# Kernel tuning notes

Hardware: AMD Instinct MI355X
Metric: run time of the kernel (lower is better)

Reference implementation:

```python
import jax, jax.numpy as jnp
import numpy as np

B, T, D, H = 8, 1024, 512, 8
DK = D // H


def setup_inputs() -> dict:
    key = jax.random.key(0)
    ks = jax.random.split(key, 6)
    s = 0.02
    return {
        "inputs": jax.random.normal(ks[0], (B, T, D), jnp.float32),
        "ln1_g": jnp.ones((D,), jnp.float32),
        "ln1_b": jnp.zeros((D,), jnp.float32),
        "ln2_g": jnp.ones((D,), jnp.float32),
        "ln2_b": jnp.zeros((D,), jnp.float32),
        "W_qkv": jax.random.normal(ks[1], (3 * D, D), jnp.float32) * s,
        "W_pos": jax.random.normal(ks[2], (D, D), jnp.float32) * s,
        "W_out": jax.random.normal(ks[3], (D, D), jnp.float32) * s,
        "b_out": jnp.zeros((D,), jnp.float32),
        "pos_bias_u": jax.random.normal(ks[4], (H, DK), jnp.float32) * s,
        "pos_bias_v": jax.random.normal(ks[5], (H, DK), jnp.float32) * s,
    }


def layer_norm(x, g, b, eps=1e-5):
    mu = jnp.mean(x, axis=-1, keepdims=True)
    var = jnp.var(x, axis=-1, keepdims=True)
    return (x - mu) * jax.lax.rsqrt(var + eps) * g + b


def rel_shift(x):
    # x: (b, h, t1, t2); Transformer-XL pad-reshape-slice relative shift
    b, h, t1, t2 = x.shape
    xp = jnp.pad(x, ((0, 0), (0, 0), (0, 0), (1, 0)))  # zero col at front
    xp = xp.reshape(b, h, t2 + 1, t1)[:, :, 1:, :]
    return xp.reshape(b, h, t1, t2)


def reference(inputs, ln1_g, ln1_b, ln2_g, ln2_b, W_qkv, W_pos, W_out, b_out,
              pos_bias_u, pos_bias_v):
    b, t, d = inputs.shape
    # PositionalEmbedding: pos_seq is the literal data values inputs[0,:,0]
    pos_seq = inputs[0, :, 0]
    inv_freq = 1.0 / (10000.0 ** (jnp.arange(0, d, 2, dtype=jnp.float32) / d))
    sin_inp = pos_seq[:, None] * inv_freq[None, :]  # (T, D/2)
    pos_emb = jnp.concatenate([jnp.sin(sin_inp), jnp.cos(sin_inp)], axis=-1)  # (T, D)
    # outer layer norm, then inner layer norm inside forward_qkv
    x = layer_norm(inputs, ln1_g, ln1_b)
    xn = layer_norm(x, ln2_g, ln2_b)
    qkv = xn @ W_qkv.T  # (B, T, 3D)
    q, k, v = jnp.split(qkv, 3, axis=-1)
    q = q.reshape(b, t, H, DK)                       # (B, T, H, DK)
    k = k.reshape(b, t, H, DK).transpose(0, 2, 1, 3)  # (B, H, T, DK)
    v = v.reshape(b, t, H, DK).transpose(0, 2, 1, 3)  # (B, H, T, DK)
    p = (pos_emb @ W_pos.T).reshape(t, H, DK)         # (T, H, DK), pos batch = 1
    qu = (q + pos_bias_u).transpose(0, 2, 1, 3)       # (B, H, T, DK)
    qv = (q + pos_bias_v).transpose(0, 2, 1, 3)
    ac = jnp.einsum('bhqd,bhkd->bhqk', qu, k)
    bd = jnp.einsum('bhqd,khd->bhqk', qv, p)
    bd = rel_shift(bd)
    scores = (ac + bd) / jnp.sqrt(jnp.float32(DK))
    attn = jax.nn.softmax(scores, axis=-1)
    out = jnp.einsum('bhqk,bhkd->bqhd', attn, v).reshape(b, t, d)
    return out @ W_out.T + b_out
```

## Files before the change

### kernel.cpp

```cpp
#include <hip/hip_runtime.h>
#include <stdint.h>

#define B_ 8
#define T_ 1024
#define D_ 512
#define H_ 8
#define DK_ 64
#define M_ (B_*T_)

#define PREP_CAST_BLKS (5 * D_ * D_ / 4 / 256)
#define PREP_POS_BLKS  (T_)
#define PREP_LN_BLKS   (M_)
#define PREP_BLKS      (PREP_CAST_BLKS + PREP_POS_BLKS + PREP_LN_BLKS)

typedef unsigned short u16;
typedef __attribute__((ext_vector_type(8))) short bf16x8;
typedef __attribute__((ext_vector_type(4))) float f32x4;

static __device__ __forceinline__ u16 f2bf(float f) {
  union { float f; unsigned u; } v; v.f = f;
  unsigned r = (v.u + 0x7fffu + ((v.u >> 16) & 1u)) >> 16;
  return (u16)r;
}
static __device__ __forceinline__ u16 f2bf_ru(float f) {
  union { float f; unsigned u; } v; v.f = f;
  return (u16)((v.u + 0x8000u) >> 16);
}
static __device__ __forceinline__ float bf2f(u16 u) {
  union { unsigned u; float f; } v; v.u = ((unsigned)u) << 16;
  return v.f;
}
static __device__ __forceinline__ void async16(const u16* g, u16* l) {
  __builtin_amdgcn_global_load_lds(
      (const __attribute__((address_space(1))) void*)g,
      (__attribute__((address_space(3))) void*)l, 16, 0, 0);
}
static __device__ __forceinline__ f32x4 mfma16(bf16x8 a, bf16x8 b, f32x4 c) {
  return __builtin_amdgcn_mfma_f32_16x16x32_bf16(a, b, c, 0, 0, 0);
}

__global__ __launch_bounds__(256)
void prep_k(const float* __restrict__ wq, const float* __restrict__ wp,
            const float* __restrict__ wo, u16* __restrict__ dq,
            u16* __restrict__ dp, u16* __restrict__ dwo,
            const float* __restrict__ x, u16* __restrict__ pe,
            const float* __restrict__ g1, const float* __restrict__ b1,
            const float* __restrict__ g2, const float* __restrict__ b2,
            u16* __restrict__ xn) {
  __shared__ float red[16];
  const int blk = blockIdx.x;
  const int t = threadIdx.x;
  if (blk < PREP_CAST_BLKS) {
    const int na = 3 * D_ * D_ / 4, nb = D_ * D_ / 4;
    int i = blk * 256 + t;
    const float* s; u16* d; int j;
    if (i < na) { s = wq; d = dq; j = i; }
    else if (i < na + nb) { s = wp; d = dp; j = i - na; }
    else { s = wo; d = dwo; j = i - na - nb; }
    float4 v = ((const float4*)s)[j];
    ushort4 o;
    o.x = f2bf(v.x); o.y = f2bf(v.y); o.z = f2bf(v.z); o.w = f2bf(v.w);
    ((ushort4*)d)[j] = o;
  } else if (blk < PREP_CAST_BLKS + PREP_POS_BLKS) {
    const int tt = blk - PREP_CAST_BLKS;
    float pos = x[(size_t)tt * D_];
    float invf = expf(-(2.f * t / (float)D_) * 9.210340371976184f);
    float ang = pos * invf;
    pe[(size_t)tt * D_ + t] = f2bf(sinf(ang));
    pe[(size_t)tt * D_ + 256 + t] = f2bf(cosf(ang));
  } else {
    const int row = blk - PREP_CAST_BLKS - PREP_POS_BLKS;
    const float2 v = *(const float2*)(x + (size_t)row * D_ + t * 2);
    float a = v.x + v.y;
    float b = v.x * v.x + v.y * v.y;
    for (int off = 32; off; off >>= 1) { a += __shfl_down(a, off, 64); b += __shfl_down(b, off, 64); }
    if ((t & 63) == 0) { red[t >> 6] = a; red[8 + (t >> 6)] = b; }
    __syncthreads();
    a = red[0] + red[1] + red[2] + red[3];
    b = red[8] + red[9] + red[10] + red[11];
    float mu = a * (1.f / D_);
    float var = b * (1.f / D_) - mu * mu;
    float rs = rsqrtf(var + 1e-5f);
    const float2 g1v = *(const float2*)(g1 + t * 2);
    const float2 b1v = *(const float2*)(b1 + t * 2);
    float y0 = (v.x - mu) * rs * g1v.x + b1v.x;
    float y1 = (v.y - mu) * rs * g1v.y + b1v.y;
    __syncthreads();
    a = y0 + y1;
    b = y0 * y0 + y1 * y1;
    for (int off = 32; off; off >>= 1) { a += __shfl_down(a, off, 64); b += __shfl_down(b, off, 64); }
    if ((t & 63) == 0) { red[t >> 6] = a; red[8 + (t >> 6)] = b; }
    __syncthreads();
    a = red[0] + red[1] + red[2] + red[3];
    b = red[8] + red[9] + red[10] + red[11];
    mu = a * (1.f / D_);
    var = b * (1.f / D_) - mu * mu;
    rs = rsqrtf(var + 1e-5f);
    const float2 g2v = *(const float2*)(g2 + t * 2);
    const float2 b2v = *(const float2*)(b2 + t * 2);
    u16* o = xn + (size_t)row * D_ + t * 2;
    o[0] = f2bf((y0 - mu) * rs * g2v.x + b2v.x);
    o[1] = f2bf((y1 - mu) * rs * g2v.y + b2v.y);
  }
}

template<int MODE>
__global__ __launch_bounds__(256, 2)
void gemm_k(const u16* __restrict__ A, const u16* __restrict__ Bw,
            int M, int N, int K,
            u16* __restrict__ o0, u16* __restrict__ o1, u16* __restrict__ o2,
            float* __restrict__ fo, const float* __restrict__ bo) {
  __shared__ u16 As[2][128 * 32];
  __shared__ u16 Bs[2][128 * 32];
  const int tid = threadIdx.x;
  const int l = tid & 63, w = tid >> 6;
  const int m0 = blockIdx.x * 128, n0 = blockIdx.y * 128;
  const int wm = (w >> 1) * 64, wn = (w & 1) * 64;
  const int nk = K >> 5;

  auto stage = [&](int bufi, int kt) {
    const int row = tid >> 2;
    const int cg = ((tid & 3) ^ ((row + (row >> 2)) & 3)) * 8;
    const u16* ga = A + (size_t)(m0 + row) * K + kt * 32 + cg;
    u16* la = &As[bufi][tid * 8];
    async16(ga, la);
    async16(ga + (size_t)64 * K, la + 64 * 32);
    const u16* gb = Bw + (size_t)(n0 + row) * K + kt * 32 + cg;
    u16* lb = &Bs[bufi][tid * 8];
    async16(gb, lb);
    async16(gb + (size_t)64 * K, lb + 64 * 32);
  };

  const int fl = (((l & 15) + ((l & 15) >> 2)) & 3);
  const int coff = ((l >> 4) ^ fl) * 8;
  const int aoff = (l & 15) * 32 + coff;

  f32x4 acc[4][4] = {};
  stage(0, 0);
  for (int kt = 0; kt < nk; ++kt) {
    __syncthreads();
    if (kt + 1 < nk) stage((kt + 1) & 1, kt + 1);
    const u16* as = As[kt & 1];
    const u16* bs = Bs[kt & 1];
    bf16x8 af[4], bfr[4];
#pragma unroll
    for (int i = 0; i < 4; ++i)
      af[i] = *(const bf16x8*)&as[(wm + i * 16) * 32 + aoff];
#pragma unroll
    for (int j = 0; j < 4; ++j)
      bfr[j] = *(const bf16x8*)&bs[(wn + j * 16) * 32 + aoff];
#pragma unroll
    for (int i = 0; i < 4; ++i)
#pragma unroll
      for (int j = 0; j < 4; ++j)
        acc[i][j] = mfma16(af[i], bfr[j], acc[i][j]);
  }

#pragma unroll
  for (int i = 0; i < 4; ++i)
#pragma unroll
    for (int j = 0; j < 4; ++j) {
      const int row0 = m0 + wm + i * 16 + ((l >> 4) << 2);
      const int col = n0 + wn + j * 16 + (l & 15);
      if (MODE == 0) {
        const int sec = col >> 9, cc = col & 511;
        const int hh = cc >> 6, dk = cc & 63;
        const int bb = row0 >> 10, t0r = row0 & 1023;
        if (sec == 2) {
          ushort4 v4;
          v4.x = f2bf(acc[i][j][0]); v4.y = f2bf(acc[i][j][1]);
          v4.z = f2bf(acc[i][j][2]); v4.w = f2bf(acc[i][j][3]);
          *(ushort4*)&o2[((size_t)(bb * H_ + hh) * DK_ + dk) * T_ + t0r] = v4;
        } else {
          u16* dst = (sec == 0) ? o0 : o1;
#pragma unroll
          for (int r = 0; r < 4; ++r)
            dst[((size_t)(bb * H_ + hh) * T_ + t0r + r) * DK_ + dk] = f2bf(acc[i][j][r]);
        }
      } else if (MODE == 1) {
        const int hh = col >> 6, dk = col & 63;
#pragma unroll
        for (int r = 0; r < 4; ++r)
          o0[((size_t)hh * T_ + row0 + r) * DK_ + dk] = f2bf(acc[i][j][r]);
      } else {
#pragma unroll
        for (int r = 0; r < 4; ++r)
          fo[(size_t)(row0 + r) * D_ + col] = acc[i][j][r] + bo[col];
      }
    }
}

__global__ __launch_bounds__(256, 3)
void attn_k(const u16* __restrict__ q, const u16* __restrict__ kb,
            const u16* __restrict__ vt, const u16* __restrict__ pb,
            const float* __restrict__ bu, const float* __restrict__ bv,
            u16* __restrict__ ao) {
  __shared__ u16 k_lds[64 * 64];
  __shared__ u16 v_lds[64 * 64];
  __shared__ u16 p_lds[128 * 64];
  __shared__ float scr[4][16 * 83];

  const int tid = threadIdx.x;
  const int l = tid & 63, w = tid >> 6;
  const int dd = blockIdx.x;
  const int bh = (dd & 7) * 8 + (dd >> 7);
  const int qb = (dd >> 3) & 15;
  const int q0 = qb * 64;
  const int b = bh >> 3, h = bh & 7;

  const u16* qB = q + (size_t)bh * T_ * DK_;
  const u16* kB = kb + (size_t)bh * T_ * DK_;
  const u16* vB = vt + (size_t)bh * DK_ * T_;
  const u16* pB = pb + (size_t)h * T_ * DK_;

  const float SCALE = 0.125f * 1.4426950408889634f;

  bf16x8 quf[2], qvf[2], qsf[2];
  {
    const float* buH = bu + h * DK_;
    const float* bvH = bv + h * DK_;
    const int row = q0 + w * 16 + (l & 15);
    const int row2 = (row + 1 < T_) ? row + 1 : T_ - 1;
    const int ko = (l >> 4) * 8;
    const bf16x8 qa0 = *(const bf16x8*)(qB + (size_t)row * DK_ + ko);
    const bf16x8 qa1 = *(const bf16x8*)(qB + (size_t)row * DK_ + ko + 32);
    const bf16x8 qs0 = *(const bf16x8*)(qB + (size_t)row2 * DK_ + ko);
    const bf16x8 qs1 = *(const bf16x8*)(qB + (size_t)row2 * DK_ + ko + 32);
#pragma unroll
    for (int jj = 0; jj < 8; ++jj) {
      float f0 = bf2f((u16)qa0[jj]), f1 = bf2f((u16)qa1[jj]);
      float g0 = bf2f((u16)qs0[jj]), g1 = bf2f((u16)qs1[jj]);
      float u0 = buH[ko + jj], u1 = buH[ko + 32 + jj];
      float v0 = bvH[ko + jj], v1 = bvH[ko + 32 + jj];
      quf[0][jj] = (short)f2bf((f0 + u0) * SCALE);
      quf[1][jj] = (short)f2bf((f1 + u1) * SCALE);
      qvf[0][jj] = (short)f2bf((f0 + v0) * SCALE);
      qvf[1][jj] = (short)f2bf((f1 + v1) * SCALE);
      qsf[0][jj] = (short)f2bf((g0 + v0) * SCALE);
      qsf[1][jj] = (short)f2bf((g1 + v1) * SCALE);
    }
  }

  f32x4 o[4] = {};
  float lrun[4] = {0.f, 0.f, 0.f, 0.f};
  float sv[4][4];

  const int rbase = 48 - w * 16;
  float* bandf = &scr[w][0];
  u16* pwv = (u16*)&scr[w][0];
  const int lrow = l & 15;
  const int c0s = ((l >> 4) ^ (l & 7)) * 8;
  const int c1s = c0s ^ 32;
  const int qrow0 = (l >> 4) * 4;

  for (int it = 0; it <= 16; ++it) {
    const int kt = it - (it > qb ? 1 : 0);
    const bool phaseU = (it > qb);
    const bool repeat = (it == qb + 1);
    const bool partial = (it == qb);
    const bool needMask = (it >= qb) && (it <= qb + 2);
    const int k0 = kt * 64;
    const int rr0 = tid >> 3;
    const int cg8 = ((tid & 7) ^ (rr0 & 7)) * 8;

    __syncthreads();
    if (!repeat) {
      const u16* g = kB + (size_t)(k0 + rr0) * DK_ + cg8;
      u16* s = &k_lds[tid * 8];
      async16(g, s);
      async16(g + 32 * DK_, s + 32 * 64);
      const u16* g2 = vB + (size_t)rr0 * T_ + k0 + cg8;
      u16* s2 = &v_lds[tid * 8];
      async16(g2, s2);
      async16(g2 + 32 * T_, s2 + 32 * 64);
    }
    {
      const int jb = phaseU ? (k0 - q0 - 65) : (T_ - 64 + k0 - q0);
#pragma unroll
      for (int i = 0; i < 4; ++i) {
        int rr = i * 32 + rr0;
        int j = jb + rr; j = j < 0 ? 0 : (j > T_ - 1 ? T_ - 1 : j);
        async16(pB + (size_t)j * DK_ + cg8, &p_lds[rr * 64 + (tid & 7) * 8]);
      }
    }
    __syncthreads();

    if (!repeat) {
      __builtin_amdgcn_s_setprio(1);
#pragma unroll
      for (int nf = 0; nf < 4; ++nf) {
        const u16* kb0 = &k_lds[(nf * 16 + lrow) * 64];
        bf16x8 b0 = *(const bf16x8*)(kb0 + c0s);
        bf16x8 b1 = *(const bf16x8*)(kb0 + c1s);
        f32x4 acs = {};
        acs = mfma16(quf[0], b0, acs);
        acs = mfma16(quf[1], b1, acs);
#pragma unroll
        for (int r = 0; r < 4; ++r) sv[nf][r] = acs[r];
      }
      __builtin_amdgcn_s_setprio(0);
    }

    {
      bf16x8 A0, A1;
      if (phaseU) { A0 = qsf[0]; A1 = qsf[1]; } else { A0 = qvf[0]; A1 = qvf[1]; }
      __builtin_amdgcn_s_setprio(1);
#pragma unroll
      for (int fu = 0; fu < 5; ++fu) {
        const u16* pb0 = &p_lds[(rbase + fu * 16 + lrow) * 64];
        bf16x8 p0 = *(const bf16x8*)(pb0 + c0s);
        bf16x8 p1 = *(const bf16x8*)(pb0 + c1s);
        f32x4 c = {};
        c = mfma16(A0, p0, c);
        c = mfma16(A1, p1, c);
#pragma unroll
        for (int r = 0; r < 4; ++r)
          bandf[(qrow0 + r) * 83 + fu * 16 + lrow] = c[r];
      }
      __builtin_amdgcn_s_setprio(0);
      if (needMask) {
        if (phaseU) {
#pragma unroll
          for (int nf = 0; nf < 4; ++nf)
#pragma unroll
            for (int r = 0; r < 4; ++r) {
              int qrow = qrow0 + r;
              int kcol = nf * 16 + lrow;
              int rel = (k0 + kcol) - (q0 + w * 16 + qrow);
              if (rel >= 2) sv[nf][r] += bandf[qrow * 83 + kcol - qrow + 15];
            }
        } else {
#pragma unroll
          for (int nf = 0; nf < 4; ++nf)
#pragma unroll
            for (int r = 0; r < 4; ++r) {
              int qrow = qrow0 + r;
              int kcol = nf * 16 + lrow;
              int rel = (k0 + kcol) - (q0 + w * 16 + qrow);
              if (rel <= 0) sv[nf][r] += bandf[qrow * 83 + kcol - qrow + 15];
            }
        }
      } else {
#pragma unroll
        for (int nf = 0; nf < 4; ++nf)
#pragma unroll
          for (int r = 0; r < 4; ++r) {
            int qrow = qrow0 + r;
            int kcol = nf * 16 + lrow;
            sv[nf][r] += bandf[qrow * 83 + kcol - qrow + 15];
          }
      }
    }

    if (!partial) {
#pragma unroll
      for (int nf = 0; nf < 4; ++nf)
#pragma unroll
        for (int r = 0; r < 4; ++r)
          sv[nf][r] = __builtin_amdgcn_exp2f(sv[nf][r]);
#pragma unroll
      for (int r = 0; r < 4; ++r)
        lrun[r] += (sv[0][r] + sv[1][r]) + (sv[2][r] + sv[3][r]);

      __builtin_amdgcn_sched_barrier(0);
#pragma unroll
      for (int nf = 0; nf < 4; ++nf)
#pragma unroll
        for (int r = 0; r < 4; ++r)
          pwv[(qrow0 + r) * 72 + nf * 16 + lrow] = f2bf_ru(sv[nf][r]);

      bf16x8 pa0 = *(const bf16x8*)&pwv[lrow * 72 + (l >> 4) * 8];
      bf16x8 pa1 = *(const bf16x8*)&pwv[lrow * 72 + 32 + (l >> 4) * 8];
      __builtin_amdgcn_s_setprio(1);
#pragma unroll
      for (int df = 0; df < 4; ++df) {
        const u16* vb2 = &v_lds[(df * 16 + lrow) * 64];
        bf16x8 v0 = *(const bf16x8*)(vb2 + c0s);
        bf16x8 v1 = *(const bf16x8*)(vb2 + c1s);
        o[df] = mfma16(pa0, v0, o[df]);
        o[df] = mfma16(pa1, v1, o[df]);
      }
      __builtin_amdgcn_s_setprio(0);
    }
  }

#pragma unroll
  for (int r = 0; r < 4; ++r) {
#pragma unroll
    for (int off = 1; off < 16; off <<= 1) lrun[r] += __shfl_xor(lrun[r], off, 64);
    lrun[r] = 1.f / lrun[r];
  }
#pragma unroll
  for (int df = 0; df < 4; ++df)
#pragma unroll
    for (int r = 0; r < 4; ++r) {
      int qq = q0 + w * 16 + (l >> 4) * 4 + r;
      int dk = df * 16 + (l & 15);
      float val = o[df][r] * lrun[r];
      ao[((size_t)b * T_ + qq) * D_ + h * DK_ + dk] = f2bf(val);
    }
}

extern "C" void kernel_launch(void* const* d_in, const int* in_sizes, int n_in,
                              void* d_out, int out_size, void* d_ws, size_t ws_size,
                              hipStream_t stream) {
  const float* inputs = (const float*)d_in[0];
  const float* ln1_g = (const float*)d_in[1];
  const float* ln1_b = (const float*)d_in[2];
  const float* ln2_g = (const float*)d_in[3];
  const float* ln2_b = (const float*)d_in[4];
  const float* W_qkv = (const float*)d_in[5];
  const float* W_pos = (const float*)d_in[6];
  const float* W_out = (const float*)d_in[7];
  const float* b_out = (const float*)d_in[8];
  const float* pbu = (const float*)d_in[9];
  const float* pbv = (const float*)d_in[10];
  float* out = (float*)d_out;

  char* ws = (char*)d_ws;
  size_t off = 0;
  auto alloc = [&](size_t bytes) {
    char* p = ws + off;
    off += (bytes + 255) & ~(size_t)255;
    return p;
  };
  u16* xn   = (u16*)alloc((size_t)M_ * D_ * 2);
  u16* wqkv = (u16*)alloc((size_t)3 * D_ * D_ * 2);
  u16* wpos = (u16*)alloc((size_t)D_ * D_ * 2);
  u16* wout = (u16*)alloc((size_t)D_ * D_ * 2);
  u16* pemb = (u16*)alloc((size_t)T_ * D_ * 2);
  u16* qB   = (u16*)alloc((size_t)M_ * D_ * 2);
  u16* kbB  = (u16*)alloc((size_t)M_ * D_ * 2);
  u16* vtB  = (u16*)alloc((size_t)M_ * D_ * 2);
  u16* pbuf = (u16*)alloc((size_t)H_ * T_ * DK_ * 2);
  u16* aoB  = (u16*)alloc((size_t)M_ * D_ * 2);
  if (ws_size < off) return;

  prep_k<<<PREP_BLKS, 256, 0, stream>>>(W_qkv, W_pos, W_out, wqkv, wpos, wout,
                                        inputs, pemb, ln1_g, ln1_b, ln2_g, ln2_b, xn);
  gemm_k<1><<<dim3(T_ / 128, D_ / 128), 256, 0, stream>>>(
      pemb, wpos, T_, D_, D_, pbuf, nullptr, nullptr, nullptr, nullptr);
  gemm_k<0><<<dim3(M_ / 128, (3 * D_) / 128), 256, 0, stream>>>(
      xn, wqkv, M_, 3 * D_, D_, qB, kbB, vtB, nullptr, nullptr);
  attn_k<<<1024, 256, 0, stream>>>(qB, kbB, vtB, pbuf, pbu, pbv, aoB);
  gemm_k<2><<<dim3(M_ / 128, D_ / 128), 256, 0, stream>>>(
      aoB, wout, M_, D_, D_, nullptr, nullptr, nullptr, out, b_out);
}
```

Measured before the change: 137.6 us.

## Prefetch K/V/P tiles via registers and shift band scores with ds_bpermute

The async global-to-LDS copies for K, V and the positional tile are replaced by register prefetch. The next iteration's tiles are loaded into registers right after the barrier and written to LDS at the start of the following iteration, so global latency overlaps with compute. The relative-shift band, which was staged through an LDS float scratch buffer, is now built with cross-lane ds_bpermute on MFMA results kept in registers. That removes the scratch writes and reads and shrinks shared memory. In exchange the kernel uses more registers, which may reduce occupancy under launch_bounds(256,3).

```diff
diff --git a/kernel.cpp b/kernel.cpp
--- a/kernel.cpp
+++ b/kernel.cpp
@@ -198,7 +198,7 @@
   __shared__ u16 k_lds[64 * 64];
   __shared__ u16 v_lds[64 * 64];
   __shared__ u16 p_lds[128 * 64];
-  __shared__ float scr[4][16 * 83];
+  __shared__ u16 pscr[4][16 * 72];
 
   const int tid = threadIdx.x;
   const int l = tid & 63, w = tid >> 6;
@@ -246,12 +246,42 @@
   float sv[4][4];
 
   const int rbase = 48 - w * 16;
-  float* bandf = &scr[w][0];
-  u16* pwv = (u16*)&scr[w][0];
+  u16* pwv = &pscr[w][0];
   const int lrow = l & 15;
   const int c0s = ((l >> 4) ^ (l & 7)) * 8;
   const int c1s = c0s ^ 32;
   const int qrow0 = (l >> 4) * 4;
+
+  int srcb[4], hi[4];
+#pragma unroll
+  for (int r = 0; r < 4; ++r) {
+    int d = lrow - qrow0 - r + 15;
+    srcb[r] = (((l >> 4) * 16 + (d & 15)) << 2);
+    hi[r] = d >> 4;
+  }
+
+  const int rr0 = tid >> 3;
+  const int cb = (tid & 7) * 8;
+  const int swz = ((tid & 7) ^ (rr0 & 7)) * 8;
+  const int wkv = rr0 * 64 + swz;
+
+  uint4 kreg0, kreg1, vreg0, vreg1, preg0, preg1, preg2, preg3;
+  auto loadKV = [&](int k0n) {
+    kreg0 = *(const uint4*)(kB + (size_t)(k0n + rr0) * DK_ + cb);
+    kreg1 = *(const uint4*)(kB + (size_t)(k0n + rr0 + 32) * DK_ + cb);
+    vreg0 = *(const uint4*)(vB + (size_t)rr0 * T_ + k0n + cb);
+    vreg1 = *(const uint4*)(vB + (size_t)(rr0 + 32) * T_ + k0n + cb);
+  };
+  auto pclamp = [&](int j) { return j < 0 ? 0 : (j > T_ - 1 ? T_ - 1 : j); };
+  auto loadP = [&](int jb) {
+    preg0 = *(const uint4*)(pB + (size_t)pclamp(jb + rr0) * DK_ + cb);
+    preg1 = *(const uint4*)(pB + (size_t)pclamp(jb + 32 + rr0) * DK_ + cb);
+    preg2 = *(const uint4*)(pB + (size_t)pclamp(jb + 64 + rr0) * DK_ + cb);
+    preg3 = *(const uint4*)(pB + (size_t)pclamp(jb + 96 + rr0) * DK_ + cb);
+  };
+
+  loadKV(0);
+  loadP(T_ - 64 - q0);
 
   for (int it = 0; it <= 16; ++it) {
     const int kt = it - (it > qb ? 1 : 0);
@@ -260,30 +290,29 @@
     const bool partial = (it == qb);
     const bool needMask = (it >= qb) && (it <= qb + 2);
     const int k0 = kt * 64;
-    const int rr0 = tid >> 3;
-    const int cg8 = ((tid & 7) ^ (rr0 & 7)) * 8;
 
     __syncthreads();
     if (!repeat) {
-      const u16* g = kB + (size_t)(k0 + rr0) * DK_ + cg8;
-      u16* s = &k_lds[tid * 8];
-      async16(g, s);
-      async16(g + 32 * DK_, s + 32 * 64);
-      const u16* g2 = vB + (size_t)rr0 * T_ + k0 + cg8;
-      u16* s2 = &v_lds[tid * 8];
-      async16(g2, s2);
-      async16(g2 + 32 * T_, s2 + 32 * 64);
-    }
-    {
-      const int jb = phaseU ? (k0 - q0 - 65) : (T_ - 64 + k0 - q0);
-#pragma unroll
-      for (int i = 0; i < 4; ++i) {
-        int rr = i * 32 + rr0;
-        int j = jb + rr; j = j < 0 ? 0 : (j > T_ - 1 ? T_ - 1 : j);
-        async16(pB + (size_t)j * DK_ + cg8, &p_lds[rr * 64 + (tid & 7) * 8]);
-      }
-    }
-    __syncthreads();
+      *(uint4*)&k_lds[wkv] = kreg0;
+      *(uint4*)&k_lds[wkv + 32 * 64] = kreg1;
+      *(uint4*)&v_lds[wkv] = vreg0;
+      *(uint4*)&v_lds[wkv + 32 * 64] = vreg1;
+    }
+    *(uint4*)&p_lds[wkv] = preg0;
+    *(uint4*)&p_lds[wkv + 32 * 64] = preg1;
+    *(uint4*)&p_lds[wkv + 64 * 64] = preg2;
+    *(uint4*)&p_lds[wkv + 96 * 64] = preg3;
+    asm volatile("s_waitcnt lgkmcnt(0)" ::: "memory");
+    __builtin_amdgcn_sched_barrier(0);
+    __builtin_amdgcn_s_barrier();
+    __builtin_amdgcn_sched_barrier(0);
+
+    if (it < 16) {
+      if (it != qb) loadKV((it + 1 - (it + 1 > qb ? 1 : 0)) * 64);
+      const bool pU = (it + 1 > qb);
+      const int ktn = it + 1 - (pU ? 1 : 0);
+      loadP(pU ? ktn * 64 - q0 - 65 : T_ - 64 + ktn * 64 - q0);
+    }
 
     if (!repeat) {
       __builtin_amdgcn_s_setprio(1);
@@ -304,51 +333,37 @@
     {
       bf16x8 A0, A1;
       if (phaseU) { A0 = qsf[0]; A1 = qsf[1]; } else { A0 = qvf[0]; A1 = qvf[1]; }
+      f32x4 c[5];
       __builtin_amdgcn_s_setprio(1);
 #pragma unroll
       for (int fu = 0; fu < 5; ++fu) {
         const u16* pb0 = &p_lds[(rbase + fu * 16 + lrow) * 64];
         bf16x8 p0 = *(const bf16x8*)(pb0 + c0s);
         bf16x8 p1 = *(const bf16x8*)(pb0 + c1s);
-        f32x4 c = {};
-        c = mfma16(A0, p0, c);
-        c = mfma16(A1, p1, c);
-#pragma unroll
-        for (int r = 0; r < 4; ++r)
-          bandf[(qrow0 + r) * 83 + fu * 16 + lrow] = c[r];
+        f32x4 cc = {};
+        cc = mfma16(A0, p0, cc);
+        cc = mfma16(A1, p1, cc);
+        c[fu] = cc;
       }
       __builtin_amdgcn_s_setprio(0);
-      if (needMask) {
-        if (phaseU) {
-#pragma unroll
-          for (int nf = 0; nf < 4; ++nf)
-#pragma unroll
-            for (int r = 0; r < 4; ++r) {
-              int qrow = qrow0 + r;
-              int kcol = nf * 16 + lrow;
-              int rel = (k0 + kcol) - (q0 + w * 16 + qrow);
-              if (rel >= 2) sv[nf][r] += bandf[qrow * 83 + kcol - qrow + 15];
-            }
-        } else {
-#pragma unroll
-          for (int nf = 0; nf < 4; ++nf)
-#pragma unroll
-            for (int r = 0; r < 4; ++r) {
-              int qrow = qrow0 + r;
-              int kcol = nf * 16 + lrow;
-              int rel = (k0 + kcol) - (q0 + w * 16 + qrow);
-              if (rel <= 0) sv[nf][r] += bandf[qrow * 83 + kcol - qrow + 15];
-            }
+#pragma unroll
+      for (int r = 0; r < 4; ++r) {
+        float rot[6];
+#pragma unroll
+        for (int fu = 0; fu < 5; ++fu)
+          rot[fu] = __int_as_float(
+              __builtin_amdgcn_ds_bpermute(srcb[r], __float_as_int(c[fu][r])));
+        rot[5] = 0.f;
+#pragma unroll
+        for (int nf = 0; nf < 4; ++nf) {
+          float bd = hi[r] ? rot[nf + 1] : rot[nf];
+          if (needMask) {
+            int rel = (k0 + nf * 16 + lrow) - (q0 + w * 16 + qrow0 + r);
+            bool ok = phaseU ? (rel >= 2) : (rel <= 0);
+            bd = ok ? bd : 0.f;
+          }
+          sv[nf][r] += bd;
         }
-      } else {
-#pragma unroll
-        for (int nf = 0; nf < 4; ++nf)
-#pragma unroll
-          for (int r = 0; r < 4; ++r) {
-            int qrow = qrow0 + r;
-            int kcol = nf * 16 + lrow;
-            sv[nf][r] += bandf[qrow * 83 + kcol - qrow + 15];
-          }
       }
     }
 
@@ -362,7 +377,6 @@
       for (int r = 0; r < 4; ++r)
         lrun[r] += (sv[0][r] + sv[1][r]) + (sv[2][r] + sv[3][r]);
 
-      __builtin_amdgcn_sched_barrier(0);
 #pragma unroll
       for (int nf = 0; nf < 4; ++nf)
 #pragma unroll
```

After: 137.4 us. No clear change (-0.1%).
